# Kernel optimization log

Measured on AMD Instinct MI355X. Metric: run time of the kernel, lower is better.

The kernel has to match this reference:

```python
import jax, jax.numpy as jnp
import numpy as np

COMMITMENT_COST = 0.25

def setup_inputs() -> dict:
    key = jax.random.key(0)
    k1, k2 = jax.random.split(key)
    inputs = jax.random.normal(k1, (32, 64, 64, 64), dtype=jnp.float32)  # NCHW, C == embedding_dim
    num_embeddings, embedding_dim = 512, 64
    # nn.Embedding weight init: uniform(-1/num_embeddings, 1/num_embeddings)
    weight = jax.random.uniform(k2, (num_embeddings, embedding_dim), dtype=jnp.float32,
                                minval=-1.0 / num_embeddings, maxval=1.0 / num_embeddings)
    return {"inputs": inputs, "weight": weight}

def reference(inputs, weight):
    B, C, H, W = inputs.shape
    K, D = weight.shape
    # permute to NHWC then flatten tokens: [B*H*W, D]
    flat = jnp.transpose(inputs, (0, 2, 3, 1)).reshape(-1, D)
    # squared L2 distances to each codebook vector: [N, K]
    distances = (jnp.sum(flat * flat, axis=1, keepdims=True)
                 - 2.0 * flat @ weight.T
                 + jnp.sum(weight * weight, axis=1))
    encoding_indices = jnp.argmin(distances, axis=1)  # [N]
    # direct gather instead of one-hot matmul (same math)
    # NOTE: original code views flat (NHWC-ordered) rows back into the NCHW
    # input shape WITHOUT inverse-permuting -- replicated faithfully here.
    quantized = weight[encoding_indices].reshape(inputs.shape)
    e_latent_loss = jnp.mean((jax.lax.stop_gradient(quantized) - inputs) ** 2)
    q_latent_loss = jnp.mean((quantized - jax.lax.stop_gradient(inputs)) ** 2)
    loss = q_latent_loss + COMMITMENT_COST * e_latent_loss
    # straight-through estimator
    quantized_st = inputs + jax.lax.stop_gradient(quantized - inputs)
    # perplexity via index counts (equivalent to mean of one-hot encodings)
    N = flat.shape[0]
    counts = jnp.zeros((K,), dtype=flat.dtype).at[encoding_indices].add(1.0)
    avg_probs = counts / N
    perplexity = jnp.exp(-jnp.sum(avg_probs * jnp.log(avg_probs + 1e-10)))
    return quantized_st, loss, perplexity
```

## Files before the change

### kernel.cpp

```cpp
#include <hip/hip_runtime.h>
#include <math.h>


#define NTOK 131072
#define KCODES 512
#define HW 4096
#define CHW 262144
#define NELEM 8388608

typedef __attribute__((ext_vector_type(8))) short short8;
typedef __attribute__((ext_vector_type(4))) float f32x4;

static __device__ __forceinline__ unsigned short f2bf(float f) {
    unsigned u = __float_as_uint(f);
    unsigned r = u + 0x7FFFu + ((u >> 16) & 1u);
    return (unsigned short)(r >> 16);
}

__global__ __launch_bounds__(512, 4) void vq_main(const float* __restrict__ in,
                                                  const float* __restrict__ w,
                                                  float* __restrict__ out,
                                                  float* __restrict__ pcounts,
                                                  double* __restrict__ ssep,
                                                  float* __restrict__ counts,
                                                  double* __restrict__ sse_acc,
                                                  const int amode) {
    __shared__ unsigned short wh[KCODES * 64];
    __shared__ float wsqp[KCODES];
    __shared__ int idxbuf[256];
    __shared__ int hist[KCODES];
    __shared__ double sred[8];

    const int tid = threadIdx.x;
    const int lane = tid & 63, wv = tid >> 6;
    const int col = lane & 15, quad = lane >> 4;
    const int ntok0 = blockIdx.x * 256;

    wsqp[tid] = 1.25f;
    hist[tid] = 0;
    __syncthreads();

    const float* gbase = in + (ntok0 >> 12) * CHW + (ntok0 & 4095) + wv * 32 + col;
    short8 ah[2][2];
    float xsq = 0.f;
#pragma unroll
    for (int it = 0; it < 8; ++it) {
        const int g = it * 512 + tid;
        const int cc = g & 15, qd = (g >> 4) & 3, ch = (g >> 6) & 1, tt = g >> 7;
        const float4* src = (const float4*)(w + (tt * 16 + cc) * 64 + ch * 32 + qd * 8);
        const float4 v0 = src[0], v1 = src[1];
        const int sub = it >> 2, c = (it >> 1) & 1, j0 = (it & 1) * 4;
        const float* gp = gbase + sub * 16 + (c * 32 + quad * 8 + j0) * HW;
        const float x0 = gp[0 * HW], x1 = gp[1 * HW], x2 = gp[2 * HW], x3 = gp[3 * HW];

        short8 hv;
        hv[0] = (short)f2bf(v0.x); hv[1] = (short)f2bf(v0.y);
        hv[2] = (short)f2bf(v0.z); hv[3] = (short)f2bf(v0.w);
        hv[4] = (short)f2bf(v1.x); hv[5] = (short)f2bf(v1.y);
        hv[6] = (short)f2bf(v1.z); hv[7] = (short)f2bf(v1.w);
        *(short8*)(wh + g * 8) = hv;
        float ws2 = v0.x * v0.x;
        ws2 = fmaf(v0.y, v0.y, ws2); ws2 = fmaf(v0.z, v0.z, ws2);
        ws2 = fmaf(v0.w, v0.w, ws2); ws2 = fmaf(v1.x, v1.x, ws2);
        ws2 = fmaf(v1.y, v1.y, ws2); ws2 = fmaf(v1.z, v1.z, ws2);
        ws2 = fmaf(v1.w, v1.w, ws2);
        atomicAdd(&wsqp[tt * 16 + cc], ws2);

        ah[sub][c][j0 + 0] = (short)f2bf(-2.0f * x0);
        ah[sub][c][j0 + 1] = (short)f2bf(-2.0f * x1);
        ah[sub][c][j0 + 2] = (short)f2bf(-2.0f * x2);
        ah[sub][c][j0 + 3] = (short)f2bf(-2.0f * x3);
        xsq = fmaf(x0, x0, xsq); xsq = fmaf(x1, x1, xsq);
        xsq = fmaf(x2, x2, xsq); xsq = fmaf(x3, x3, xsq);
    }
    __syncthreads();

    unsigned runkey[2][4];
#pragma unroll
    for (int sub = 0; sub < 2; ++sub)
#pragma unroll
        for (int r = 0; r < 4; ++r) runkey[sub][r] = 0xFFFFFFFFu;

#pragma unroll 1
    for (int t = 0; t < 32; ++t) {
        const unsigned short* ph = wh + t * 1024 + quad * 128 + col * 8;
        const short8 b0 = *(const short8*)ph;
        const short8 b1 = *(const short8*)(ph + 512);
        const int code = t * 16 + col;
        const float seed = wsqp[code];
#pragma unroll
        for (int sub = 0; sub < 2; ++sub) {
            f32x4 acc = {seed, seed, seed, seed};
            acc = __builtin_amdgcn_mfma_f32_16x16x32_bf16(ah[sub][0], b0, acc, 0, 0, 0);
            acc = __builtin_amdgcn_mfma_f32_16x16x32_bf16(ah[sub][1], b1, acc, 0, 0, 0);
#pragma unroll
            for (int r = 0; r < 4; ++r) {
                const unsigned key = (__float_as_uint(acc[r]) << 9) | code;
                runkey[sub][r] = key < runkey[sub][r] ? key : runkey[sub][r];
            }
        }
    }

#pragma unroll
    for (int s = 1; s < 16; s <<= 1)
#pragma unroll
        for (int sub = 0; sub < 2; ++sub)
#pragma unroll
            for (int r = 0; r < 4; ++r) {
                const unsigned o = __shfl_xor(runkey[sub][r], s, 64);
                runkey[sub][r] = o < runkey[sub][r] ? o : runkey[sub][r];
            }

    float dsum = 0.f;
    if (col == 0) {
#pragma unroll
        for (int sub = 0; sub < 2; ++sub)
#pragma unroll
            for (int r = 0; r < 4; ++r) {
                const unsigned key = runkey[sub][r];
                idxbuf[wv * 32 + sub * 16 + quad * 4 + r] = (int)(key & 511u);
                dsum += __uint_as_float((key >> 9) | 0x3F800000u) - 1.25f;
            }
    }
    float contrib = xsq + dsum;
#pragma unroll
    for (int off = 32; off > 0; off >>= 1) contrib += __shfl_down(contrib, off, 64);
    if (lane == 0) sred[wv] = (double)contrib;
    __syncthreads();

    if (tid < 256) atomicAdd(&hist[idxbuf[tid]], 1);

#pragma unroll
    for (int p = 0; p < 2; ++p) {
        const int tl = p * 16 + (lane >> 2), q = lane & 3;
        const int n = ntok0 + wv * 32 + tl;
        const int bidx = idxbuf[wv * 32 + tl];
        const float4* wr = (const float4*)(w + bidx * 64 + q * 16);
        float4* op = (float4*)(out + n * 64 + q * 16);
#pragma unroll
        for (int i = 0; i < 4; ++i) op[i] = wr[i];
    }
    __syncthreads();

    if (!amode) {
        pcounts[(blockIdx.x << 9) + tid] = (float)hist[tid];
        if (tid == 0) {
            double s = sred[0];
#pragma unroll
            for (int i = 1; i < 8; ++i) s += sred[i];
            ssep[blockIdx.x] = s;
        }
    } else {
        const int h = hist[tid];
        if (h) atomicAdd(&counts[tid], (float)h);
        if (tid == 0) {
            double s = sred[0];
#pragma unroll
            for (int i = 1; i < 8; ++i) s += sred[i];
            atomicAdd(sse_acc, s);
        }
    }
}

__global__ __launch_bounds__(512) void vq_final_p(const float* __restrict__ pcounts,
                                                  const double* __restrict__ ssep,
                                                  float* __restrict__ out) {
    __shared__ float part[4][512];
    __shared__ double red[512];
    __shared__ double sred[512];
    const int t = threadIdx.x;
    const int q = t >> 7, c4 = (t & 127) << 2;

    const float4* base = (const float4*)pcounts + (q << 14) + (c4 >> 2);
    float4 s = {0.f, 0.f, 0.f, 0.f};
#pragma unroll 16
    for (int b = 0; b < 128; ++b) {
        const float4 v = base[b << 7];
        s.x += v.x; s.y += v.y; s.z += v.z; s.w += v.w;
    }
    *(float4*)&part[q][c4] = s;
    sred[t] = ssep[t];
    __syncthreads();

    const float cnt = part[0][t] + part[1][t] + part[2][t] + part[3][t];
    const double p = (double)cnt / (double)NTOK;
    red[t] = p * log(p + 1e-10);
    __syncthreads();
#pragma unroll
    for (int st = 256; st > 0; st >>= 1) {
        if (t < st) { red[t] += red[t + st]; sred[t] += sred[t + st]; }
        __syncthreads();
    }
    if (t == 0) {
        out[NELEM] = (float)((sred[0] / (double)NELEM) * 1.25);
        out[NELEM + 1] = (float)exp(-red[0]);
    }
}

__global__ __launch_bounds__(512) void vq_final_a(const float* __restrict__ counts,
                                                  const double* __restrict__ sse_acc,
                                                  float* __restrict__ out) {
    __shared__ double red[512];
    const int k = threadIdx.x;
    const double p = (double)counts[k] / (double)NTOK;
    red[k] = p * log(p + 1e-10);
    __syncthreads();
#pragma unroll
    for (int st = 256; st > 0; st >>= 1) {
        if (k < st) red[k] += red[k + st];
        __syncthreads();
    }
    if (k == 0) {
        out[NELEM] = (float)((*sse_acc / (double)NELEM) * 1.25);
        out[NELEM + 1] = (float)exp(-red[0]);
    }
}

extern "C" void kernel_launch(void* const* d_in, const int* in_sizes, int n_in,
                              void* d_out, int out_size, void* d_ws, size_t ws_size,
                              hipStream_t stream) {
    const float* in = (const float*)d_in[0];
    const float* w = (const float*)d_in[1];
    float* out = (float*)d_out;
    char* ws = (char*)d_ws;

    const size_t need = (size_t)512 * 512 * 4 + 512 * 8;
    if (ws_size >= need) {
        float* pcounts = (float*)ws;
        double* ssep = (double*)(ws + (size_t)512 * 512 * 4);
        vq_main<<<512, 512, 0, stream>>>(in, w, out, pcounts, ssep,
                                         nullptr, nullptr, 0);
        vq_final_p<<<1, 512, 0, stream>>>(pcounts, ssep, out);
    } else {
        float* counts = (float*)ws;
        double* sse_acc = (double*)(ws + 2048);
        hipMemsetAsync(ws, 0, 2056, stream);
        vq_main<<<512, 512, 0, stream>>>(in, w, out, nullptr, nullptr,
                                         counts, sse_acc, 1);
        vq_final_a<<<1, 512, 0, stream>>>(counts, sse_acc, out);
    }
}
```

Measured before the change: 117.4 us.

## Pre-pack bf16 codebook once and stream B operands from global memory

A new single-block kernel converts the codebook to bf16 in MFMA fragment order and precomputes squared norms once per call. The main kernel no longer converts the codebook into shared memory per block, which removes 64KB of LDS, the conversion work, the LDS float atomics and a barrier. B fragments are now read straight from global memory (mostly L2 hits), with the t loop unrolled 4x. Per-block histogram partials shrink to 16-bit, and the histogram update skips one block barrier. The cost is an extra kernel launch, plus global/L2 latency on the inner loop in place of LDS reads.

```diff
diff --git a/kernel.cpp b/kernel.cpp
--- a/kernel.cpp
+++ b/kernel.cpp
@@ -10,6 +10,7 @@
 
 typedef __attribute__((ext_vector_type(8))) short short8;
 typedef __attribute__((ext_vector_type(4))) float f32x4;
+typedef __attribute__((ext_vector_type(4))) unsigned short u16x4;
 
 static __device__ __forceinline__ unsigned short f2bf(float f) {
     unsigned u = __float_as_uint(f);
@@ -17,15 +18,48 @@
     return (unsigned short)(r >> 16);
 }
 
-__global__ __launch_bounds__(512, 4) void vq_main(const float* __restrict__ in,
+__global__ __launch_bounds__(512) void vq_pack(const float* __restrict__ w,
+                                               unsigned short* __restrict__ wpack,
+                                               float* __restrict__ wsqf) {
+    const int code = threadIdx.x;
+    const int tt = code >> 4, cc = code & 15;
+    const float4* src = (const float4*)(w + code * 64);
+    float4 v[16];
+#pragma unroll
+    for (int i = 0; i < 16; ++i) v[i] = src[i];
+    float s = 0.f;
+#pragma unroll
+    for (int i = 0; i < 16; ++i) {
+        s = fmaf(v[i].x, v[i].x, s); s = fmaf(v[i].y, v[i].y, s);
+        s = fmaf(v[i].z, v[i].z, s); s = fmaf(v[i].w, v[i].w, s);
+    }
+    wsqf[code] = 1.25f + s;
+#pragma unroll
+    for (int ch = 0; ch < 2; ++ch)
+#pragma unroll
+        for (int qd = 0; qd < 4; ++qd) {
+            const int g = tt * 128 + ch * 64 + qd * 16 + cc;
+            const int e0 = ch * 8 + qd * 2;
+            const float4 a = v[e0], b = v[e0 + 1];
+            short8 hv;
+            hv[0] = (short)f2bf(a.x); hv[1] = (short)f2bf(a.y);
+            hv[2] = (short)f2bf(a.z); hv[3] = (short)f2bf(a.w);
+            hv[4] = (short)f2bf(b.x); hv[5] = (short)f2bf(b.y);
+            hv[6] = (short)f2bf(b.z); hv[7] = (short)f2bf(b.w);
+            *(short8*)(wpack + g * 8) = hv;
+        }
+}
+
+__global__ __launch_bounds__(512, 4) void vq_scan(const float* __restrict__ in,
                                                   const float* __restrict__ w,
+                                                  const unsigned short* __restrict__ wpack,
+                                                  const float* __restrict__ wsqf,
                                                   float* __restrict__ out,
-                                                  float* __restrict__ pcounts,
+                                                  unsigned short* __restrict__ pcounts,
                                                   double* __restrict__ ssep,
                                                   float* __restrict__ counts,
                                                   double* __restrict__ sse_acc,
                                                   const int amode) {
-    __shared__ unsigned short wh[KCODES * 64];
     __shared__ float wsqp[KCODES];
     __shared__ int idxbuf[256];
     __shared__ int hist[KCODES];
@@ -36,7 +70,7 @@
     const int col = lane & 15, quad = lane >> 4;
     const int ntok0 = blockIdx.x * 256;
 
-    wsqp[tid] = 1.25f;
+    wsqp[tid] = wsqf[tid];
     hist[tid] = 0;
     __syncthreads();
 
@@ -45,27 +79,9 @@
     float xsq = 0.f;
 #pragma unroll
     for (int it = 0; it < 8; ++it) {
-        const int g = it * 512 + tid;
-        const int cc = g & 15, qd = (g >> 4) & 3, ch = (g >> 6) & 1, tt = g >> 7;
-        const float4* src = (const float4*)(w + (tt * 16 + cc) * 64 + ch * 32 + qd * 8);
-        const float4 v0 = src[0], v1 = src[1];
         const int sub = it >> 2, c = (it >> 1) & 1, j0 = (it & 1) * 4;
         const float* gp = gbase + sub * 16 + (c * 32 + quad * 8 + j0) * HW;
         const float x0 = gp[0 * HW], x1 = gp[1 * HW], x2 = gp[2 * HW], x3 = gp[3 * HW];
-
-        short8 hv;
-        hv[0] = (short)f2bf(v0.x); hv[1] = (short)f2bf(v0.y);
-        hv[2] = (short)f2bf(v0.z); hv[3] = (short)f2bf(v0.w);
-        hv[4] = (short)f2bf(v1.x); hv[5] = (short)f2bf(v1.y);
-        hv[6] = (short)f2bf(v1.z); hv[7] = (short)f2bf(v1.w);
-        *(short8*)(wh + g * 8) = hv;
-        float ws2 = v0.x * v0.x;
-        ws2 = fmaf(v0.y, v0.y, ws2); ws2 = fmaf(v0.z, v0.z, ws2);
-        ws2 = fmaf(v0.w, v0.w, ws2); ws2 = fmaf(v1.x, v1.x, ws2);
-        ws2 = fmaf(v1.y, v1.y, ws2); ws2 = fmaf(v1.z, v1.z, ws2);
-        ws2 = fmaf(v1.w, v1.w, ws2);
-        atomicAdd(&wsqp[tt * 16 + cc], ws2);
-
         ah[sub][c][j0 + 0] = (short)f2bf(-2.0f * x0);
         ah[sub][c][j0 + 1] = (short)f2bf(-2.0f * x1);
         ah[sub][c][j0 + 2] = (short)f2bf(-2.0f * x2);
@@ -73,19 +89,18 @@
         xsq = fmaf(x0, x0, xsq); xsq = fmaf(x1, x1, xsq);
         xsq = fmaf(x2, x2, xsq); xsq = fmaf(x3, x3, xsq);
     }
-    __syncthreads();
-
+
+    const unsigned short* pb = wpack + quad * 128 + col * 8;
     unsigned runkey[2][4];
 #pragma unroll
     for (int sub = 0; sub < 2; ++sub)
 #pragma unroll
         for (int r = 0; r < 4; ++r) runkey[sub][r] = 0xFFFFFFFFu;
 
-#pragma unroll 1
+#pragma unroll 4
     for (int t = 0; t < 32; ++t) {
-        const unsigned short* ph = wh + t * 1024 + quad * 128 + col * 8;
-        const short8 b0 = *(const short8*)ph;
-        const short8 b1 = *(const short8*)(ph + 512);
+        const short8 b0 = *(const short8*)(pb + t * 1024);
+        const short8 b1 = *(const short8*)(pb + t * 1024 + 512);
         const int code = t * 16 + col;
         const float seed = wsqp[code];
 #pragma unroll
@@ -126,9 +141,8 @@
 #pragma unroll
     for (int off = 32; off > 0; off >>= 1) contrib += __shfl_down(contrib, off, 64);
     if (lane == 0) sred[wv] = (double)contrib;
-    __syncthreads();
-
-    if (tid < 256) atomicAdd(&hist[idxbuf[tid]], 1);
+
+    if (lane < 32) atomicAdd(&hist[idxbuf[wv * 32 + lane]], 1);
 
 #pragma unroll
     for (int p = 0; p < 2; ++p) {
@@ -143,7 +157,7 @@
     __syncthreads();
 
     if (!amode) {
-        pcounts[(blockIdx.x << 9) + tid] = (float)hist[tid];
+        pcounts[(blockIdx.x << 9) + tid] = (unsigned short)hist[tid];
         if (tid == 0) {
             double s = sred[0];
 #pragma unroll
@@ -162,7 +176,7 @@
     }
 }
 
-__global__ __launch_bounds__(512) void vq_final_p(const float* __restrict__ pcounts,
+__global__ __launch_bounds__(512) void vq_final_p(const unsigned short* __restrict__ pcounts,
                                                   const double* __restrict__ ssep,
                                                   float* __restrict__ out) {
     __shared__ float part[4][512];
@@ -171,12 +185,13 @@
     const int t = threadIdx.x;
     const int q = t >> 7, c4 = (t & 127) << 2;
 
-    const float4* base = (const float4*)pcounts + (q << 14) + (c4 >> 2);
+    const u16x4* base = (const u16x4*)pcounts + (q << 14) + (c4 >> 2);
     float4 s = {0.f, 0.f, 0.f, 0.f};
 #pragma unroll 16
     for (int b = 0; b < 128; ++b) {
-        const float4 v = base[b << 7];
-        s.x += v.x; s.y += v.y; s.z += v.z; s.w += v.w;
+        const u16x4 v = base[b << 7];
+        s.x += (float)v[0]; s.y += (float)v[1];
+        s.z += (float)v[2]; s.w += (float)v[3];
     }
     *(float4*)&part[q][c4] = s;
     sred[t] = ssep[t];
@@ -224,18 +239,29 @@
     float* out = (float*)d_out;
     char* ws = (char*)d_ws;
 
-    const size_t need = (size_t)512 * 512 * 4 + 512 * 8;
-    if (ws_size >= need) {
-        float* pcounts = (float*)ws;
-        double* ssep = (double*)(ws + (size_t)512 * 512 * 4);
-        vq_main<<<512, 512, 0, stream>>>(in, w, out, pcounts, ssep,
+    const size_t WP = 0;
+    const size_t WQ = 65536;
+    const size_t PC = WQ + 2048;
+    const size_t SSo = PC + (size_t)512 * 512 * 2;
+    const size_t need_full = SSo + 512 * 8;
+    const size_t need_min = PC + 2048 + 8;
+
+    unsigned short* wpack = (unsigned short*)(ws + WP);
+    float* wsqf = (float*)(ws + WQ);
+
+    if (ws_size >= need_full) {
+        unsigned short* pcounts = (unsigned short*)(ws + PC);
+        double* ssep = (double*)(ws + SSo);
+        vq_pack<<<1, 512, 0, stream>>>(w, wpack, wsqf);
+        vq_scan<<<512, 512, 0, stream>>>(in, w, wpack, wsqf, out, pcounts, ssep,
                                          nullptr, nullptr, 0);
         vq_final_p<<<1, 512, 0, stream>>>(pcounts, ssep, out);
-    } else {
-        float* counts = (float*)ws;
-        double* sse_acc = (double*)(ws + 2048);
-        hipMemsetAsync(ws, 0, 2056, stream);
-        vq_main<<<512, 512, 0, stream>>>(in, w, out, nullptr, nullptr,
+    } else if (ws_size >= need_min) {
+        float* counts = (float*)(ws + PC);
+        double* sse_acc = (double*)(ws + PC + 2048);
+        (void)hipMemsetAsync(ws + PC, 0, 2056, stream);
+        vq_pack<<<1, 512, 0, stream>>>(w, wpack, wsqf);
+        vq_scan<<<512, 512, 0, stream>>>(in, w, wpack, wsqf, out, nullptr, nullptr,
                                          counts, sse_acc, 1);
         vq_final_a<<<1, 512, 0, stream>>>(counts, sse_acc, out);
     }
```

New measurement: 115.7 us. No clear change (-1.4%).
